# Kernel tuning notes

Measured on AMD Instinct MI355X. Metric: run time of the kernel, lower is better.

Reference implementation:

```python
import jax, jax.numpy as jnp
import numpy as np

# Problem dims (see shape_source)
M_MACH = 50          # n_machines
N_JOBS = 100         # n_jobs
MT_BITS = 4          # machine_time_bits (capped at 4)
JS_BITS = 2          # job_status_bits (capped at 2)
OBS = M_MACH + N_JOBS + M_MACH * N_JOBS          # 5150
F = M_MACH * MT_BITS + N_JOBS * JS_BITS + M_MACH * N_JOBS  # 5400 total binary features
A = 32               # number of actions (one Tsetlin machine each)
C = 1000             # clauses per TM (min(nr_of_clauses, 1000))
INIT = 16            # TA-state include/exclude threshold


def setup_inputs() -> dict:
    key = jax.random.key(0)
    k1, k2, k3, k4, k5 = jax.random.split(key, 5)
    # state = [machine_times | job_status | op_status]; op_status is binary in the env
    machine_times = jax.random.uniform(k1, (M_MACH,), dtype=jnp.float32) * 100.0
    job_status = jax.random.uniform(k2, (N_JOBS,), dtype=jnp.float32)
    op_status = jax.random.randint(k3, (M_MACH * N_JOBS,), 0, 2).astype(jnp.float32)
    state = jnp.concatenate([machine_times, job_status, op_status])
    # TA states in [1, 32); >16 means literal is included. int8 as in the torch module.
    ta_state = jax.random.randint(k4, (A, C, 2, F), 1, 32).astype(jnp.int8)
    # clause signs in {+1, -1}
    clause_sign = (2 * jax.random.randint(k5, (A, C), 0, 2) - 1).astype(jnp.int8)
    return {"state": state, "ta_state": ta_state, "clause_sign": clause_sign}


def _binary_encode(state):
    """JSSPFeatureTransformer.transform: state -> [F] int32 binary features."""
    mt = state[:M_MACH]
    mx = jnp.max(mt)
    safe_mx = jnp.where(mx > 0, mx, jnp.float32(1.0))
    # if max_time == 0 the torch code leaves these bits at zero; where() matches that
    norm = jnp.where(mx > 0, mt / safe_mx * (2 ** MT_BITS - 1), 0.0).astype(jnp.int32)
    mt_bits = ((norm[:, None] // (2 ** jnp.arange(MT_BITS, dtype=jnp.int32))) % 2).reshape(-1)
    js = state[M_MACH:M_MACH + N_JOBS]
    status = jnp.minimum((js * (2 ** JS_BITS - 1)).astype(jnp.int32), 2 ** JS_BITS - 1)
    js_bits = ((status[:, None] // (2 ** jnp.arange(JS_BITS, dtype=jnp.int32))) % 2).reshape(-1)
    op_bits = state[M_MACH + N_JOBS:].astype(jnp.int32)
    return jnp.concatenate([mt_bits, js_bits, op_bits])  # [F]


def reference(state, ta_state, clause_sign):
    feats = _binary_encode(state)                         # [F] int32 in {0,1}
    ta = ta_state.astype(jnp.int8)
    include = ta[:, :, 0, :] > INIT                       # [A,C,F]
    exclude = ta[:, :, 1, :] > INIT                       # [A,C,F]
    f0 = (feats == 0)[None, None, :]
    f1 = (feats == 1)[None, None, :]
    violations = jnp.any((include & f0) | (exclude & f1), axis=-1)  # [A,C]
    clause_out = (~violations).astype(jnp.int32)          # [A,C]
    # pos_sum - neg_sum == sum(clause_out * sign) with sign in {+1,-1}
    q_values = jnp.sum(clause_out * clause_sign.astype(jnp.int32), axis=-1)
    return q_values.astype(jnp.float32)                   # [A]
```

## Files before the change

kernel.cpp:

```cpp
#include <hip/hip_runtime.h>
#include <stdint.h>

#define M_MACH 50
#define N_JOBS 100
#define MT_BITS 4
#define JS_BITS 2
#define NFEAT (M_MACH * MT_BITS + N_JOBS * JS_BITS + M_MACH * N_JOBS)
#define A_DIM 32
#define C_DIM 1000
#define INIT_T 16

__global__ void encode_kernel(const float* __restrict__ state,
                              uint8_t* __restrict__ feats,
                              float* __restrict__ out) {
    const int tid = threadIdx.x;

    if (tid < A_DIM) out[tid] = 0.0f;

    __shared__ float smax;
    if (tid < 64) {
        float v = (tid < M_MACH) ? state[tid] : -1.0f;
        #pragma unroll
        for (int off = 32; off > 0; off >>= 1)
            v = fmaxf(v, __shfl_down(v, off, 64));
        if (tid == 0) smax = v;
    }
    __syncthreads();
    const float mx = smax;

    for (int f = tid; f < NFEAT; f += blockDim.x) {
        uint8_t bit;
        if (f < M_MACH * MT_BITS) {
            const int i = f >> 2;
            const int k = f & 3;
            int norm = 0;
            if (mx > 0.0f) {
                norm = (int)((state[i] / mx) * 15.0f);
            }
            bit = (uint8_t)((norm >> k) & 1);
        } else if (f < M_MACH * MT_BITS + N_JOBS * JS_BITS) {
            const int rel = f - M_MACH * MT_BITS;
            const int j = rel >> 1;
            const int k = rel & 1;
            int status = (int)(state[M_MACH + j] * 3.0f);
            if (status > 3) status = 3;
            bit = (uint8_t)((status >> k) & 1);
        } else {
            const int i = f - (M_MACH * MT_BITS + N_JOBS * JS_BITS);
            bit = (uint8_t)((int)state[M_MACH + N_JOBS + i]);
        }
        feats[f] = bit;
    }
}

__global__ __launch_bounds__(256) void clause_kernel(
    const int8_t* __restrict__ ta,
    const int8_t* __restrict__ sign,
    const uint8_t* __restrict__ feats,
    float* __restrict__ out) {
    const int lane = threadIdx.x & 63;
    const int wid  = threadIdx.x >> 6;
    const int gwave = blockIdx.x * 4 + wid;
    const int nwaves = gridDim.x * 4;

    for (int q = gwave; q < A_DIM * C_DIM; q += nwaves) {
        const int a = q / C_DIM;
        const int8_t* base = ta + (size_t)q * (2 * NFEAT);

        bool violated = false;
        for (int f0 = 0; f0 < NFEAT; f0 += 64) {
            const int f = f0 + lane;
            bool v = false;
            if (f < NFEAT) {
                const int p = feats[f];
                v = base[p * NFEAT + f] > INIT_T;
            }
            if (__any(v)) { violated = true; break; }
        }

        if (!violated && lane == 0) {
            atomicAdd(&out[a], (float)sign[q]);
        }
    }
}

extern "C" void kernel_launch(void* const* d_in, const int* in_sizes, int n_in,
                              void* d_out, int out_size, void* d_ws, size_t ws_size,
                              hipStream_t stream) {
    const float*  state = (const float*)d_in[0];
    const int8_t* ta    = (const int8_t*)d_in[1];
    const int8_t* sign  = (const int8_t*)d_in[2];
    float* out = (float*)d_out;
    uint8_t* feats = (uint8_t*)d_ws;

    encode_kernel<<<1, 256, 0, stream>>>(state, feats, out);

    clause_kernel<<<2048, 256, 0, stream>>>(ta, sign, feats, out);
}
```

Before: 13.81 us.

## Fuse feature encoding into clause kernel with one wave per clause

```diff
diff --git a/kernel.cpp b/kernel.cpp
--- a/kernel.cpp
+++ b/kernel.cpp
@@ -3,85 +3,62 @@
 
 #define M_MACH 50
 #define N_JOBS 100
-#define MT_BITS 4
-#define JS_BITS 2
-#define NFEAT (M_MACH * MT_BITS + N_JOBS * JS_BITS + M_MACH * N_JOBS)
+#define NFEAT 5400
 #define A_DIM 32
 #define C_DIM 1000
 #define INIT_T 16
+#define WAVES_PER_BLOCK 8
 
-__global__ void encode_kernel(const float* __restrict__ state,
-                              uint8_t* __restrict__ feats,
-                              float* __restrict__ out) {
-    const int tid = threadIdx.x;
-
-    if (tid < A_DIM) out[tid] = 0.0f;
-
-    __shared__ float smax;
-    if (tid < 64) {
-        float v = (tid < M_MACH) ? state[tid] : -1.0f;
-        #pragma unroll
-        for (int off = 32; off > 0; off >>= 1)
-            v = fmaxf(v, __shfl_down(v, off, 64));
-        if (tid == 0) smax = v;
-    }
-    __syncthreads();
-    const float mx = smax;
-
-    for (int f = tid; f < NFEAT; f += blockDim.x) {
-        uint8_t bit;
-        if (f < M_MACH * MT_BITS) {
-            const int i = f >> 2;
-            const int k = f & 3;
-            int norm = 0;
-            if (mx > 0.0f) {
-                norm = (int)((state[i] / mx) * 15.0f);
-            }
-            bit = (uint8_t)((norm >> k) & 1);
-        } else if (f < M_MACH * MT_BITS + N_JOBS * JS_BITS) {
-            const int rel = f - M_MACH * MT_BITS;
-            const int j = rel >> 1;
-            const int k = rel & 1;
-            int status = (int)(state[M_MACH + j] * 3.0f);
-            if (status > 3) status = 3;
-            bit = (uint8_t)((status >> k) & 1);
-        } else {
-            const int i = f - (M_MACH * MT_BITS + N_JOBS * JS_BITS);
-            bit = (uint8_t)((int)state[M_MACH + N_JOBS + i]);
-        }
-        feats[f] = bit;
-    }
-}
-
-__global__ __launch_bounds__(256) void clause_kernel(
+__global__ __launch_bounds__(512) void fused_clause_kernel(
+    const float* __restrict__ state,
     const int8_t* __restrict__ ta,
     const int8_t* __restrict__ sign,
-    const uint8_t* __restrict__ feats,
     float* __restrict__ out) {
     const int lane = threadIdx.x & 63;
     const int wid  = threadIdx.x >> 6;
-    const int gwave = blockIdx.x * 4 + wid;
-    const int nwaves = gridDim.x * 4;
+    const int q    = blockIdx.x * WAVES_PER_BLOCK + wid;
+    const int8_t* base = ta + (size_t)q * (2 * NFEAT);
 
-    for (int q = gwave; q < A_DIM * C_DIM; q += nwaves) {
-        const int a = q / C_DIM;
-        const int8_t* base = ta + (size_t)q * (2 * NFEAT);
+    const int in0 = base[lane];
+    const int ex0 = base[NFEAT + lane];
 
-        bool violated = false;
-        for (int f0 = 0; f0 < NFEAT; f0 += 64) {
-            const int f = f0 + lane;
-            bool v = false;
-            if (f < NFEAT) {
-                const int p = feats[f];
-                v = base[p * NFEAT + f] > INIT_T;
+    const float v0 = (lane < M_MACH) ? state[lane] : -1.0f;
+    float mx = v0;
+    #pragma unroll
+    for (int off = 1; off < 64; off <<= 1)
+        mx = fmaxf(mx, __shfl_xor(mx, off, 64));
+
+    const float s_i = __shfl(v0, lane >> 2, 64);
+    const int norm = (mx > 0.0f) ? (int)((s_i / mx) * 15.0f) : 0;
+    const int bit  = (norm >> (lane & 3)) & 1;
+
+    const bool v = ((bit ? ex0 : in0) > INIT_T);
+    if (__any(v)) return;
+
+    for (int f0 = 64; f0 < NFEAT; f0 += 64) {
+        const int f = f0 + lane;
+        bool vv = false;
+        if (f < NFEAT) {
+            int b;
+            if (f < M_MACH * 4) {
+                const int i = f >> 2;
+                const int n2 = (mx > 0.0f) ? (int)((state[i] / mx) * 15.0f) : 0;
+                b = (n2 >> (f & 3)) & 1;
+            } else if (f < M_MACH * 4 + N_JOBS * 2) {
+                const int rel = f - M_MACH * 4;
+                const int j = rel >> 1;
+                int st = (int)(state[M_MACH + j] * 3.0f);
+                if (st > 3) st = 3;
+                b = (st >> (rel & 1)) & 1;
+            } else {
+                b = (int)state[M_MACH + N_JOBS + (f - (M_MACH*4 + N_JOBS*2))];
             }
-            if (__any(v)) { violated = true; break; }
+            vv = ((b ? base[NFEAT + f] : base[f]) > INIT_T);
         }
+        if (__any(vv)) return;
+    }
 
-        if (!violated && lane == 0) {
-            atomicAdd(&out[a], (float)sign[q]);
-        }
-    }
+    if (lane == 0) atomicAdd(&out[q / C_DIM], (float)sign[q]);
 }
 
 extern "C" void kernel_launch(void* const* d_in, const int* in_sizes, int n_in,
@@ -91,9 +68,8 @@
     const int8_t* ta    = (const int8_t*)d_in[1];
     const int8_t* sign  = (const int8_t*)d_in[2];
     float* out = (float*)d_out;
-    uint8_t* feats = (uint8_t*)d_ws;
 
-    encode_kernel<<<1, 256, 0, stream>>>(state, feats, out);
+    hipMemsetAsync(out, 0, out_size * sizeof(float), stream);
 
-    clause_kernel<<<2048, 256, 0, stream>>>(ta, sign, feats, out);
+    fused_clause_kernel<<<4000, 512, 0, stream>>>(state, ta, sign, out);
 }
```

After: 13.89 us. No clear change (+0.6%).
